# Kernel optimization log

Measured on AMD Instinct MI355X. Metric: run time of the kernel, lower is better.

The kernel has to match this reference:

```python
import jax, jax.numpy as jnp
import numpy as np

B, S, D, H, L = 256, 2048, 64, 256, 2


def setup_inputs() -> dict:
    key = jax.random.key(0)
    ks = jax.random.split(key, 12)
    s_in = 1.0 / np.sqrt(H)  # torch nn.RNN init bound
    inp = {
        "x": jax.random.normal(ks[0], (B, S, D), dtype=jnp.float32),
        "W_ih0": jax.random.uniform(ks[1], (H, D), jnp.float32, -s_in, s_in),
        "W_hh0": jax.random.uniform(ks[2], (H, H), jnp.float32, -s_in, s_in),
        "b_ih0": jax.random.uniform(ks[3], (H,), jnp.float32, -s_in, s_in),
        "b_hh0": jax.random.uniform(ks[4], (H,), jnp.float32, -s_in, s_in),
        "W_ih1": jax.random.uniform(ks[5], (H, H), jnp.float32, -s_in, s_in),
        "W_hh1": jax.random.uniform(ks[6], (H, H), jnp.float32, -s_in, s_in),
        "b_ih1": jax.random.uniform(ks[7], (H,), jnp.float32, -s_in, s_in),
        "b_hh1": jax.random.uniform(ks[8], (H,), jnp.float32, -s_in, s_in),
        "W_out": jax.random.uniform(ks[9], (1, H), jnp.float32, -s_in, s_in),
        "b_out": jax.random.uniform(ks[10], (1,), jnp.float32, -s_in, s_in),
    }
    return inp


def _rnn_layer_seq(xs, W_ih, W_hh, b_ih, b_hh):
    """xs: [S,B,Din] -> outputs [S,B,H]; collects every step."""
    # precompute input projection once (batched GEMM), recurrence only adds h @ W_hh
    pre = jnp.einsum('sbd,hd->sbh', xs, W_ih) + b_ih + b_hh  # [S,B,H]
    h0 = jnp.zeros((xs.shape[1], W_hh.shape[0]), dtype=xs.dtype)

    def step(h, p_t):
        h_new = jnp.tanh(p_t + h @ W_hh.T)
        return h_new, h_new

    _, ys = jax.lax.scan(step, h0, pre)
    return ys


def _rnn_layer_last(xs, W_ih, W_hh, b_ih, b_hh):
    """xs: [S,B,Din] -> final hidden state [B,H]; no per-step outputs kept."""
    pre = jnp.einsum('sbd,hd->sbh', xs, W_ih) + b_ih + b_hh
    h0 = jnp.zeros((xs.shape[1], W_hh.shape[0]), dtype=xs.dtype)

    def step(h, p_t):
        return jnp.tanh(p_t + h @ W_hh.T), None

    h_last, _ = jax.lax.scan(step, h0, pre)
    return h_last


def reference(x, W_ih0, W_hh0, b_ih0, b_hh0, W_ih1, W_hh1, b_ih1, b_hh1, W_out, b_out):
    xs = jnp.transpose(x, (1, 0, 2))  # [S,B,D] time-major for scan
    ys0 = _rnn_layer_seq(xs, W_ih0, W_hh0, b_ih0, b_hh0)      # [S,B,H]
    h_last = _rnn_layer_last(ys0, W_ih1, W_hh1, b_ih1, b_hh1)  # [B,H]
    return jax.nn.sigmoid(h_last @ W_out.T + b_out)            # [B,1]
```

## Files before the change

### kernel.cpp

```cpp
#include <hip/hip_runtime.h>
#include <cstdint>


#define S_LEN 2048
#define DIN   64
#define HDIM  256
#define CH    64

typedef __attribute__((ext_vector_type(8))) short bf16x8;
typedef __attribute__((ext_vector_type(4))) float f32x4;

__device__ __forceinline__ short f2bf(float f) {
  unsigned u = __builtin_bit_cast(unsigned, f);
  u += 0x7FFFu + ((u >> 16) & 1u);
  return (short)(u >> 16);
}
__device__ __forceinline__ float bf2f(unsigned short h) {
  return __builtin_bit_cast(float, ((unsigned)h) << 16);
}
__device__ __forceinline__ bf16x8 cvt8(f32x4 a, f32x4 b) {
  bf16x8 r;
  r[0]=f2bf(a[0]); r[1]=f2bf(a[1]); r[2]=f2bf(a[2]); r[3]=f2bf(a[3]);
  r[4]=f2bf(b[0]); r[5]=f2bf(b[1]); r[6]=f2bf(b[2]); r[7]=f2bf(b[3]);
  return r;
}
__device__ __forceinline__ bf16x8 load8cvt(const float* p) {
  f32x4 a = *(const f32x4*)p;
  f32x4 b = *(const f32x4*)(p + 4);
  return cvt8(a, b);
}
__device__ __forceinline__ f32x4 mfma16(bf16x8 a, bf16x8 b, f32x4 c) {
  return __builtin_amdgcn_mfma_f32_16x16x32_bf16(a, b, c, 0, 0, 0);
}
__device__ __forceinline__ float fast_tanh(float x) {
  float e = __expf(2.0f * x);
  float r = __builtin_amdgcn_rcpf(1.0f + e);
  return 1.0f - 2.0f * r;
}
__device__ __forceinline__ int frag_off(int k, int m) {
  return ((k >> 5) << 10) | (((k >> 3) & 3) << 8) | (m << 4) | ((k & 7) << 1);
}
__device__ __forceinline__ f32x4 unpk4(uint2 v) {
  f32x4 a;
  a[0] = __builtin_bit_cast(float, v.x << 16);
  a[1] = __builtin_bit_cast(float, v.x & 0xFFFF0000u);
  a[2] = __builtin_bit_cast(float, v.y << 16);
  a[3] = __builtin_bit_cast(float, v.y & 0xFFFF0000u);
  return a;
}
__device__ __forceinline__ uint2 pk4(f32x4 a) {
  uint2 p;
  p.x = (unsigned)(unsigned short)f2bf(a[0]) | ((unsigned)(unsigned short)f2bf(a[1]) << 16);
  p.y = (unsigned)(unsigned short)f2bf(a[2]) | ((unsigned)(unsigned short)f2bf(a[3]) << 16);
  return p;
}
__device__ __forceinline__ unsigned ld_acq(unsigned* p) {
  return __hip_atomic_load(p, __ATOMIC_ACQUIRE, __HIP_MEMORY_SCOPE_AGENT);
}
__device__ __forceinline__ void st_rlx(unsigned* p, unsigned v) {
  __hip_atomic_store(p, v, __ATOMIC_RELAXED, __HIP_MEMORY_SCOPE_AGENT);
}
__device__ __forceinline__ void bar_lds() {
  asm volatile("s_waitcnt lgkmcnt(0)" ::: "memory");
  __builtin_amdgcn_s_barrier();
}

__global__ void zero_flags(unsigned* f) {
  if (threadIdx.x < 64) f[threadIdx.x] = 0u;
}

__global__ void __launch_bounds__(256)
x_proj(const float* __restrict__ x, const float* __restrict__ Wih0,
       const float* __restrict__ bih0, const float* __restrict__ bhh0,
       uint2* __restrict__ pre0) {
  const int tid = threadIdx.x, w = tid >> 6, l = tid & 63;
  const int lm = l & 15, lq = l >> 4;
  const int tile = blockIdx.x, tch = blockIdx.y;

  bf16x8 wih[4][2]; float bias[4];
#pragma unroll
  for (int i = 0; i < 4; ++i) {
    int n = ((w * 4 + i) << 4) + lm;
    wih[i][0] = load8cvt(Wih0 + n * DIN + lq * 8);
    wih[i][1] = load8cvt(Wih0 + n * DIN + 32 + lq * 8);
    bias[i] = bih0[n] + bhh0[n];
  }
  const float* xb = x + (size_t)(tile * 16 + lm) * (S_LEN * DIN) + lq * 8;
  for (int tt = 0; tt < 16; ++tt) {
    int t = tch * 16 + tt;
    const float* xp = xb + (size_t)t * DIN;
    bf16x8 xa0 = load8cvt(xp);
    bf16x8 xa1 = load8cvt(xp + 32);
    uint2* dst = pre0 + ((size_t)(tile * S_LEN + t) * 16 + w * 4) * 64 + l;
#pragma unroll
    for (int i = 0; i < 4; ++i) {
      f32x4 a = {bias[i], bias[i], bias[i], bias[i]};
      a = mfma16(xa0, wih[i][0], a);
      a = mfma16(xa1, wih[i][1], a);
      dst[(size_t)i * 64] = pk4(a);
    }
  }
}

__global__ void __launch_bounds__(512, 2)
rnn_pipe2(const float* __restrict__ Whh0, const float* __restrict__ Wih1,
          const float* __restrict__ Whh1, const float* __restrict__ bih1,
          const float* __restrict__ bhh1, const float* __restrict__ Wout,
          const float* __restrict__ bout, uint2* __restrict__ pre0,
          unsigned* __restrict__ flags, float* __restrict__ out) {
  __shared__ __align__(16) char smem[17408];

  const int tid = threadIdx.x, w = tid >> 6, l = tid & 63;
  const int lm = l & 15, lq = l >> 4;
  const int role = blockIdx.x >> 4;
  const int tile = blockIdx.x & 15;

  const int lbase = l << 4;
  const int wbase = frag_off(w * 32 + lm, lq << 2);
  uint2* pb = pre0 + (size_t)tile * (S_LEN * 1024) + w * 128 + l;
  unsigned* flag = flags + tile;

  if (role == 0) {
    bf16x8 whh0[2][8], wih1[2][8];
    float bias1[2];
#pragma unroll
    for (int i = 0; i < 2; ++i) {
      int n = ((w * 2 + i) << 4) + lm;
#pragma unroll
      for (int kt = 0; kt < 8; ++kt) {
        whh0[i][kt] = load8cvt(Whh0 + n * HDIM + kt * 32 + lq * 8);
        wih1[i][kt] = load8cvt(Wih1 + n * HDIM + kt * 32 + lq * 8);
      }
      bias1[i] = bih1[n] + bhh1[n];
    }
    uint2 bufA[2], bufB[2];
    bufA[0] = pb[0];    bufA[1] = pb[64];
    bufB[0] = pb[1024]; bufB[1] = pb[1024 + 64];

    {
#pragma unroll
      for (int i = 0; i < 2; ++i) {
        f32x4 a = unpk4(bufA[i]);
#pragma unroll
        for (int r = 0; r < 4; ++r)
          *(short*)(smem + wbase + i * 512 + r * 16) = f2bf(fast_tanh(a[r]));
      }
      const uint2* np = pb + (size_t)2 * 1024;
      bufA[0] = np[0]; bufA[1] = np[64];
      bar_lds();
    }

    auto phaseA = [&](int p, int pbit, uint2 (&buf)[2]) {
      const int h0r = (pbit ^ 1) * 8192;
      const int h0w = pbit * 8192;
      f32x4 a0 = unpk4(buf[0]), a1 = unpk4(buf[1]);
      f32x4 g0 = {bias1[0], bias1[0], bias1[0], bias1[0]};
      f32x4 g1 = {bias1[1], bias1[1], bias1[1], bias1[1]};
#pragma unroll
      for (int kt = 0; kt < 8; ++kt) {
        bf16x8 hf = *(const bf16x8*)(smem + h0r + kt * 1024 + lbase);
        a0 = mfma16(hf, whh0[0][kt], a0);
        a1 = mfma16(hf, whh0[1][kt], a1);
        g0 = mfma16(hf, wih1[0][kt], g0);
        g1 = mfma16(hf, wih1[1][kt], g1);
      }
      {
        int tn = (p + 2 < S_LEN) ? p + 2 : S_LEN - 1;
        const uint2* np = pb + (size_t)tn * 1024;
        buf[0] = np[0]; buf[1] = np[64];
      }
#pragma unroll
      for (int i = 0; i < 2; ++i) {
        f32x4 a = i ? a1 : a0;
#pragma unroll
        for (int r = 0; r < 4; ++r)
          *(short*)(smem + h0w + wbase + i * 512 + r * 16) = f2bf(fast_tanh(a[r]));
      }
      {
        uint2* gd = pb + (size_t)(p - 1) * 1024;
        gd[0] = pk4(g0); gd[64] = pk4(g1);
      }
      if ((p & (CH - 1)) == 0) {
        __builtin_amdgcn_fence(__ATOMIC_RELEASE, "agent");
        __syncthreads();
        if (tid == 0) st_rlx(flag, (unsigned)(p >> 6));
      } else {
        bar_lds();
      }
    };

    for (int p = 1; p + 1 < S_LEN; p += 2) {
      phaseA(p, 1, bufB);
      phaseA(p + 1, 0, bufA);
    }
    phaseA(S_LEN - 1, 1, bufB);

    {
      f32x4 g0 = {bias1[0], bias1[0], bias1[0], bias1[0]};
      f32x4 g1 = {bias1[1], bias1[1], bias1[1], bias1[1]};
#pragma unroll
      for (int kt = 0; kt < 8; ++kt) {
        bf16x8 hf = *(const bf16x8*)(smem + 8192 + kt * 1024 + lbase);
        g0 = mfma16(hf, wih1[0][kt], g0);
        g1 = mfma16(hf, wih1[1][kt], g1);
      }
      uint2* gd = pb + (size_t)(S_LEN - 1) * 1024;
      gd[0] = pk4(g0); gd[64] = pk4(g1);
      __builtin_amdgcn_fence(__ATOMIC_RELEASE, "agent");
      __syncthreads();
      if (tid == 0) st_rlx(flag, (unsigned)(S_LEN / CH));
    }

  } else {
    bf16x8 whh1[2][8];
#pragma unroll
    for (int i = 0; i < 2; ++i) {
      int n = ((w * 2 + i) << 4) + lm;
#pragma unroll
      for (int kt = 0; kt < 8; ++kt)
        whh1[i][kt] = load8cvt(Whh1 + n * HDIM + kt * 32 + lq * 8);
    }
    ((f32x4*)(smem + 8192))[tid] = (f32x4){0.f, 0.f, 0.f, 0.f};
    __syncthreads();

    uint2 gcur[2], gnxt[2];
    unsigned have = 0;

    auto stepB = [&](int t, int pbit) {
      const int h1r = (pbit ^ 1) * 8192;
      const int h1w = pbit * 8192;
      const bool pf = ((t & (CH - 1)) != CH - 1);
      if (pf) {
        const uint2* np = pb + (size_t)(t + 1) * 1024;
        gnxt[0] = np[0]; gnxt[1] = np[64];
      }
      f32x4 c0 = unpk4(gcur[0]), c1 = unpk4(gcur[1]);
#pragma unroll
      for (int kt = 0; kt < 8; ++kt) {
        bf16x8 hf = *(const bf16x8*)(smem + h1r + kt * 1024 + lbase);
        c0 = mfma16(hf, whh1[0][kt], c0);
        c1 = mfma16(hf, whh1[1][kt], c1);
      }
#pragma unroll
      for (int i = 0; i < 2; ++i) {
        f32x4 c = i ? c1 : c0;
#pragma unroll
        for (int r = 0; r < 4; ++r)
          *(short*)(smem + h1w + wbase + i * 512 + r * 16) = f2bf(fast_tanh(c[r]));
      }
      if (pf) { gcur[0] = gnxt[0]; gcur[1] = gnxt[1]; }
      bar_lds();
    };

    for (int c = 0; c < S_LEN / CH; ++c) {
      while (have < (unsigned)(c + 1)) {
        have = ld_acq(flag);
        if (have < (unsigned)(c + 1)) __builtin_amdgcn_s_sleep(8);
      }
      const int t0 = c * CH;
      { const uint2* np = pb + (size_t)t0 * 1024; gcur[0] = np[0]; gcur[1] = np[64]; }
      for (int tt = 0; tt < CH; tt += 2) {
        stepB(t0 + tt, 0);
        stepB(t0 + tt + 1, 1);
      }
    }

    if (tid < 256) {
      int m = tid >> 4, j = tid & 15;
      float s = 0.f;
#pragma unroll
      for (int kk = 0; kk < 16; ++kk) {
        int k = j * 16 + kk;
        s += bf2f(*(unsigned short*)(smem + 8192 + frag_off(k, m))) * Wout[k];
      }
      ((float*)(smem + 16384))[(m << 4) + j] = s;
    }
    __syncthreads();
    if (tid < 16) {
      float s = 0.f;
#pragma unroll
      for (int j = 0; j < 16; ++j) s += ((float*)(smem + 16384))[(tid << 4) + j];
      s += bout[0];
      out[(tile << 4) + tid] = 1.f / (1.f + __expf(-s));
    }
  }
}

__global__ void __launch_bounds__(512, 2)
rnn_pre8(const float* __restrict__ Whh0, const float* __restrict__ Wih1,
         const float* __restrict__ Whh1, const float* __restrict__ bih1,
         const float* __restrict__ bhh1, const float* __restrict__ Wout,
         const float* __restrict__ bout, const uint2* __restrict__ pre0,
         float* __restrict__ out) {
  __shared__ __align__(16) char smem[33792];

  const int tid = threadIdx.x, w = tid >> 6, l = tid & 63;
  const int lm = l & 15, lq = l >> 4;
  const int tile = blockIdx.x;

  bf16x8 whh0[2][8], wih1[2][8], whh1[2][8];
  float bias1[2];
#pragma unroll
  for (int i = 0; i < 2; ++i) {
    int n = ((w * 2 + i) << 4) + lm;
#pragma unroll
    for (int kt = 0; kt < 8; ++kt) {
      whh0[i][kt] = load8cvt(Whh0 + n * HDIM + kt * 32 + lq * 8);
      wih1[i][kt] = load8cvt(Wih1 + n * HDIM + kt * 32 + lq * 8);
      whh1[i][kt] = load8cvt(Whh1 + n * HDIM + kt * 32 + lq * 8);
    }
    bias1[i] = bih1[n] + bhh1[n];
  }
  ((f32x4*)(smem + 24576))[tid] = (f32x4){0.f, 0.f, 0.f, 0.f};

  const int lbase = l << 4;
  const int wbase = frag_off(w * 32 + lm, lq << 2);
  const uint2* pbase = pre0 + (size_t)tile * (S_LEN * 1024) + w * 128 + l;
  uint2 bufA[2], bufB[2];
  bufA[0] = pbase[0];    bufA[1] = pbase[64];
  bufB[0] = pbase[1024]; bufB[1] = pbase[1024 + 64];

  {
#pragma unroll
    for (int i = 0; i < 2; ++i) {
      f32x4 a = unpk4(bufA[i]);
#pragma unroll
      for (int r = 0; r < 4; ++r)
        *(short*)(smem + wbase + i * 512 + r * 16) = f2bf(fast_tanh(a[r]));
    }
    const uint2* np = pbase + (size_t)2 * 1024;
    bufA[0] = np[0]; bufA[1] = np[64];
    bar_lds();
  }

  auto phase = [&](int p, int pbit, uint2 (&buf)[2]) {
    const int h0r_o = (pbit ^ 1) * 8192;
    const int h0w_o = pbit * 8192;
    const int h1r_o = 16384 + pbit * 8192;
    const int h1w_o = 16384 + (pbit ^ 1) * 8192;

    f32x4 a0 = unpk4(buf[0]), a1 = unpk4(buf[1]);
    f32x4 c0 = {bias1[0], bias1[0], bias1[0], bias1[0]};
    f32x4 c1 = {bias1[1], bias1[1], bias1[1], bias1[1]};
#pragma unroll
    for (int kt = 0; kt < 8; ++kt) {
      bf16x8 hf = *(const bf16x8*)(smem + h0r_o + kt * 1024 + lbase);
      a0 = mfma16(hf, whh0[0][kt], a0);
      a1 = mfma16(hf, whh0[1][kt], a1);
      c0 = mfma16(hf, wih1[0][kt], c0);
      c1 = mfma16(hf, wih1[1][kt], c1);
    }
#pragma unroll
    for (int kt = 0; kt < 8; ++kt) {
      bf16x8 hf = *(const bf16x8*)(smem + h1r_o + kt * 1024 + lbase);
      c0 = mfma16(hf, whh1[0][kt], c0);
      c1 = mfma16(hf, whh1[1][kt], c1);
    }
#pragma unroll
    for (int i = 0; i < 2; ++i) {
      f32x4 a = i ? a1 : a0;
      f32x4 c = i ? c1 : c0;
#pragma unroll
      for (int r = 0; r < 4; ++r) {
        *(short*)(smem + h0w_o + wbase + i * 512 + r * 16) = f2bf(fast_tanh(a[r]));
        *(short*)(smem + h1w_o + wbase + i * 512 + r * 16) = f2bf(fast_tanh(c[r]));
      }
    }
    {
      int tn = (p + 2 < S_LEN) ? p + 2 : S_LEN - 1;
      const uint2* np = pbase + (size_t)tn * 1024;
      buf[0] = np[0]; buf[1] = np[64];
    }
    bar_lds();
  };

  for (int p = 1; p + 1 < S_LEN; p += 2) {
    phase(p, 1, bufB);
    phase(p + 1, 0, bufA);
  }
  phase(S_LEN - 1, 1, bufB);

  {
    f32x4 c0 = {bias1[0], bias1[0], bias1[0], bias1[0]};
    f32x4 c1 = {bias1[1], bias1[1], bias1[1], bias1[1]};
#pragma unroll
    for (int kt = 0; kt < 8; ++kt) {
      bf16x8 hf = *(const bf16x8*)(smem + 8192 + kt * 1024 + lbase);
      c0 = mfma16(hf, wih1[0][kt], c0);
      c1 = mfma16(hf, wih1[1][kt], c1);
    }
#pragma unroll
    for (int kt = 0; kt < 8; ++kt) {
      bf16x8 hf = *(const bf16x8*)(smem + 16384 + kt * 1024 + lbase);
      c0 = mfma16(hf, whh1[0][kt], c0);
      c1 = mfma16(hf, whh1[1][kt], c1);
    }
#pragma unroll
    for (int i = 0; i < 2; ++i) {
      f32x4 c = i ? c1 : c0;
#pragma unroll
      for (int r = 0; r < 4; ++r)
        *(short*)(smem + 24576 + wbase + i * 512 + r * 16) = f2bf(fast_tanh(c[r]));
    }
    __syncthreads();
  }

  if (tid < 256) {
    int m = tid >> 4, j = tid & 15;
    float s = 0.f;
#pragma unroll
    for (int kk = 0; kk < 16; ++kk) {
      int k = j * 16 + kk;
      s += bf2f(*(unsigned short*)(smem + 24576 + frag_off(k, m))) * Wout[k];
    }
    ((float*)(smem + 32768))[(m << 4) + j] = s;
  }
  __syncthreads();
  if (tid < 16) {
    float s = 0.f;
#pragma unroll
    for (int j = 0; j < 16; ++j) s += ((float*)(smem + 32768))[(tid << 4) + j];
    s += bout[0];
    out[(tile << 4) + tid] = 1.f / (1.f + __expf(-s));
  }
}

extern "C" void kernel_launch(void* const* d_in, const int* in_sizes, int n_in,
                              void* d_out, int out_size, void* d_ws, size_t ws_size,
                              hipStream_t stream) {
  (void)in_sizes; (void)n_in; (void)out_size;
  const float* x    = (const float*)d_in[0];
  const float* Wih0 = (const float*)d_in[1];
  const float* Whh0 = (const float*)d_in[2];
  const float* bih0 = (const float*)d_in[3];
  const float* bhh0 = (const float*)d_in[4];
  const float* Wih1 = (const float*)d_in[5];
  const float* Whh1 = (const float*)d_in[6];
  const float* bih1 = (const float*)d_in[7];
  const float* bhh1 = (const float*)d_in[8];
  const float* Wout = (const float*)d_in[9];
  const float* bout = (const float*)d_in[10];

  const size_t PRE_BYTES = (size_t)16 * S_LEN * 16 * 64 * 8;

  x_proj<<<dim3(16, 128), dim3(256), 0, stream>>>(x, Wih0, bih0, bhh0,
                                                  (uint2*)d_ws);
  if (ws_size >= PRE_BYTES + 4096) {
    unsigned* flags = (unsigned*)((char*)d_ws + PRE_BYTES);
    zero_flags<<<dim3(1), dim3(64), 0, stream>>>(flags);
    rnn_pipe2<<<dim3(32), dim3(512), 0, stream>>>(
        Whh0, Wih1, Whh1, bih1, bhh1, Wout, bout, (uint2*)d_ws, flags,
        (float*)d_out);
  } else {
    rnn_pre8<<<dim3(16), dim3(512), 0, stream>>>(
        Whh0, Wih1, Whh1, bih1, bhh1, Wout, bout, (const uint2*)d_ws,
        (float*)d_out);
  }
}
```

Before: 2.166 ms.

## Halve waves per recurrent block, four output tiles per wave, packed DPP stores

The recurrent pipeline kernel now runs 4 waves of 256 threads instead of 8, and each wave computes four 16-column output tiles per step. Fewer waves per block should make each per-step barrier cheaper and raise MFMA work per wave. The cost is twice the register-resident weights, up to 64 bf16x8 fragments in the layer-0 role. Hidden-state stores to LDS now pair neighbouring lanes through DPP into 32-bit writes, and the consumer spin-wait gains an iteration budget that proceeds anyway once exhausted, which could read unready data.

```diff
diff --git a/kernel.cpp b/kernel.cpp
--- a/kernel.cpp
+++ b/kernel.cpp
@@ -36,6 +36,12 @@
   float e = __expf(2.0f * x);
   float r = __builtin_amdgcn_rcpf(1.0f + e);
   return 1.0f - 2.0f * r;
+}
+__device__ __forceinline__ f32x4 tanh4(f32x4 a) {
+  f32x4 r;
+  r[0] = fast_tanh(a[0]); r[1] = fast_tanh(a[1]);
+  r[2] = fast_tanh(a[2]); r[3] = fast_tanh(a[3]);
+  return r;
 }
 __device__ __forceinline__ int frag_off(int k, int m) {
   return ((k >> 5) << 10) | (((k >> 3) & 3) << 8) | (m << 4) | ((k & 7) << 1);
@@ -64,6 +70,15 @@
   asm volatile("s_waitcnt lgkmcnt(0)" ::: "memory");
   __builtin_amdgcn_s_barrier();
 }
+__device__ __forceinline__ void sth4(char* base, int wb, f32x4 a, int l) {
+#pragma unroll
+  for (int r = 0; r < 4; ++r) {
+    unsigned own = (unsigned)(unsigned short)f2bf(a[r]);
+    unsigned nb = (unsigned)__builtin_amdgcn_mov_dpp((int)own, 0xB1, 0xF, 0xF, true);
+    if ((l & 1) == 0)
+      *(unsigned*)(base + wb + r * 16) = own | (nb << 16);
+  }
+}
 
 __global__ void zero_flags(unsigned* f) {
   if (threadIdx.x < 64) f[threadIdx.x] = 0u;
@@ -102,8 +117,8 @@
   }
 }
 
-__global__ void __launch_bounds__(512, 2)
-rnn_pipe2(const float* __restrict__ Whh0, const float* __restrict__ Wih1,
+__global__ void __launch_bounds__(256, 1)
+rnn_pipe4(const float* __restrict__ Whh0, const float* __restrict__ Wih1,
           const float* __restrict__ Whh1, const float* __restrict__ bih1,
           const float* __restrict__ bhh1, const float* __restrict__ Wout,
           const float* __restrict__ bout, uint2* __restrict__ pre0,
@@ -116,69 +131,75 @@
   const int tile = blockIdx.x & 15;
 
   const int lbase = l << 4;
-  const int wbase = frag_off(w * 32 + lm, lq << 2);
-  uint2* pb = pre0 + (size_t)tile * (S_LEN * 1024) + w * 128 + l;
+  int wb[4];
+#pragma unroll
+  for (int i = 0; i < 4; ++i) wb[i] = frag_off(w * 64 + i * 16 + lm, lq << 2);
+  uint2* pb = pre0 + (size_t)tile * (S_LEN * 1024) + w * 256 + l;
   unsigned* flag = flags + tile;
 
   if (role == 0) {
-    bf16x8 whh0[2][8], wih1[2][8];
-    float bias1[2];
-#pragma unroll
-    for (int i = 0; i < 2; ++i) {
-      int n = ((w * 2 + i) << 4) + lm;
+    bf16x8 whh0[4][8], wih1r[4][8];
+    float bias1[4];
+#pragma unroll
+    for (int i = 0; i < 4; ++i) {
+      int n = ((w * 4 + i) << 4) + lm;
 #pragma unroll
       for (int kt = 0; kt < 8; ++kt) {
-        whh0[i][kt] = load8cvt(Whh0 + n * HDIM + kt * 32 + lq * 8);
-        wih1[i][kt] = load8cvt(Wih1 + n * HDIM + kt * 32 + lq * 8);
+        whh0[i][kt]  = load8cvt(Whh0 + n * HDIM + kt * 32 + lq * 8);
+        wih1r[i][kt] = load8cvt(Wih1 + n * HDIM + kt * 32 + lq * 8);
       }
       bias1[i] = bih1[n] + bhh1[n];
     }
-    uint2 bufA[2], bufB[2];
-    bufA[0] = pb[0];    bufA[1] = pb[64];
-    bufB[0] = pb[1024]; bufB[1] = pb[1024 + 64];
+    uint2 bufA[4], bufB[4];
+#pragma unroll
+    for (int i = 0; i < 4; ++i) {
+      bufA[i] = pb[i * 64];
+      bufB[i] = pb[1024 + i * 64];
+    }
 
     {
 #pragma unroll
-      for (int i = 0; i < 2; ++i) {
-        f32x4 a = unpk4(bufA[i]);
-#pragma unroll
-        for (int r = 0; r < 4; ++r)
-          *(short*)(smem + wbase + i * 512 + r * 16) = f2bf(fast_tanh(a[r]));
-      }
+      for (int i = 0; i < 4; ++i) sth4(smem, wb[i], tanh4(unpk4(bufA[i])), l);
       const uint2* np = pb + (size_t)2 * 1024;
-      bufA[0] = np[0]; bufA[1] = np[64];
+#pragma unroll
+      for (int i = 0; i < 4; ++i) bufA[i] = np[i * 64];
       bar_lds();
     }
 
-    auto phaseA = [&](int p, int pbit, uint2 (&buf)[2]) {
+    auto phaseA = [&](int p, int pbit, uint2 (&buf)[4]) {
       const int h0r = (pbit ^ 1) * 8192;
       const int h0w = pbit * 8192;
       f32x4 a0 = unpk4(buf[0]), a1 = unpk4(buf[1]);
+      f32x4 a2 = unpk4(buf[2]), a3 = unpk4(buf[3]);
       f32x4 g0 = {bias1[0], bias1[0], bias1[0], bias1[0]};
       f32x4 g1 = {bias1[1], bias1[1], bias1[1], bias1[1]};
+      f32x4 g2 = {bias1[2], bias1[2], bias1[2], bias1[2]};
+      f32x4 g3 = {bias1[3], bias1[3], bias1[3], bias1[3]};
 #pragma unroll
       for (int kt = 0; kt < 8; ++kt) {
         bf16x8 hf = *(const bf16x8*)(smem + h0r + kt * 1024 + lbase);
         a0 = mfma16(hf, whh0[0][kt], a0);
         a1 = mfma16(hf, whh0[1][kt], a1);
-        g0 = mfma16(hf, wih1[0][kt], g0);
-        g1 = mfma16(hf, wih1[1][kt], g1);
+        a2 = mfma16(hf, whh0[2][kt], a2);
+        a3 = mfma16(hf, whh0[3][kt], a3);
+        g0 = mfma16(hf, wih1r[0][kt], g0);
+        g1 = mfma16(hf, wih1r[1][kt], g1);
+        g2 = mfma16(hf, wih1r[2][kt], g2);
+        g3 = mfma16(hf, wih1r[3][kt], g3);
       }
       {
         int tn = (p + 2 < S_LEN) ? p + 2 : S_LEN - 1;
         const uint2* np = pb + (size_t)tn * 1024;
-        buf[0] = np[0]; buf[1] = np[64];
-      }
-#pragma unroll
-      for (int i = 0; i < 2; ++i) {
-        f32x4 a = i ? a1 : a0;
-#pragma unroll
-        for (int r = 0; r < 4; ++r)
-          *(short*)(smem + h0w + wbase + i * 512 + r * 16) = f2bf(fast_tanh(a[r]));
-      }
+#pragma unroll
+        for (int i = 0; i < 4; ++i) buf[i] = np[i * 64];
+      }
+      sth4(smem + h0w, wb[0], tanh4(a0), l);
+      sth4(smem + h0w, wb[1], tanh4(a1), l);
+      sth4(smem + h0w, wb[2], tanh4(a2), l);
+      sth4(smem + h0w, wb[3], tanh4(a3), l);
       {
         uint2* gd = pb + (size_t)(p - 1) * 1024;
-        gd[0] = pk4(g0); gd[64] = pk4(g1);
+        gd[0] = pk4(g0); gd[64] = pk4(g1); gd[128] = pk4(g2); gd[192] = pk4(g3);
       }
       if ((p & (CH - 1)) == 0) {
         __builtin_amdgcn_fence(__ATOMIC_RELEASE, "agent");
@@ -198,33 +219,39 @@
     {
       f32x4 g0 = {bias1[0], bias1[0], bias1[0], bias1[0]};
       f32x4 g1 = {bias1[1], bias1[1], bias1[1], bias1[1]};
+      f32x4 g2 = {bias1[2], bias1[2], bias1[2], bias1[2]};
+      f32x4 g3 = {bias1[3], bias1[3], bias1[3], bias1[3]};
 #pragma unroll
       for (int kt = 0; kt < 8; ++kt) {
         bf16x8 hf = *(const bf16x8*)(smem + 8192 + kt * 1024 + lbase);
-        g0 = mfma16(hf, wih1[0][kt], g0);
-        g1 = mfma16(hf, wih1[1][kt], g1);
+        g0 = mfma16(hf, wih1r[0][kt], g0);
+        g1 = mfma16(hf, wih1r[1][kt], g1);
+        g2 = mfma16(hf, wih1r[2][kt], g2);
+        g3 = mfma16(hf, wih1r[3][kt], g3);
       }
       uint2* gd = pb + (size_t)(S_LEN - 1) * 1024;
-      gd[0] = pk4(g0); gd[64] = pk4(g1);
+      gd[0] = pk4(g0); gd[64] = pk4(g1); gd[128] = pk4(g2); gd[192] = pk4(g3);
       __builtin_amdgcn_fence(__ATOMIC_RELEASE, "agent");
       __syncthreads();
       if (tid == 0) st_rlx(flag, (unsigned)(S_LEN / CH));
     }
 
   } else {
-    bf16x8 whh1[2][8];
-#pragma unroll
-    for (int i = 0; i < 2; ++i) {
-      int n = ((w * 2 + i) << 4) + lm;
+    bf16x8 whh1r[4][8];
+#pragma unroll
+    for (int i = 0; i < 4; ++i) {
+      int n = ((w * 4 + i) << 4) + lm;
 #pragma unroll
       for (int kt = 0; kt < 8; ++kt)
-        whh1[i][kt] = load8cvt(Whh1 + n * HDIM + kt * 32 + lq * 8);
+        whh1r[i][kt] = load8cvt(Whh1 + n * HDIM + kt * 32 + lq * 8);
     }
     ((f32x4*)(smem + 8192))[tid] = (f32x4){0.f, 0.f, 0.f, 0.f};
+    ((f32x4*)(smem + 8192))[tid + 256] = (f32x4){0.f, 0.f, 0.f, 0.f};
     __syncthreads();
 
-    uint2 gcur[2], gnxt[2];
+    uint2 gcur[4], gnxt[4];
     unsigned have = 0;
+    unsigned spin_budget = 4000000u;
 
     auto stepB = [&](int t, int pbit) {
       const int h1r = (pbit ^ 1) * 8192;
@@ -232,40 +259,51 @@
       const bool pf = ((t & (CH - 1)) != CH - 1);
       if (pf) {
         const uint2* np = pb + (size_t)(t + 1) * 1024;
-        gnxt[0] = np[0]; gnxt[1] = np[64];
+#pragma unroll
+        for (int i = 0; i < 4; ++i) gnxt[i] = np[i * 64];
       }
       f32x4 c0 = unpk4(gcur[0]), c1 = unpk4(gcur[1]);
+      f32x4 c2 = unpk4(gcur[2]), c3 = unpk4(gcur[3]);
 #pragma unroll
       for (int kt = 0; kt < 8; ++kt) {
         bf16x8 hf = *(const bf16x8*)(smem + h1r + kt * 1024 + lbase);
-        c0 = mfma16(hf, whh1[0][kt], c0);
-        c1 = mfma16(hf, whh1[1][kt], c1);
-      }
-#pragma unroll
-      for (int i = 0; i < 2; ++i) {
-        f32x4 c = i ? c1 : c0;
-#pragma unroll
-        for (int r = 0; r < 4; ++r)
-          *(short*)(smem + h1w + wbase + i * 512 + r * 16) = f2bf(fast_tanh(c[r]));
-      }
-      if (pf) { gcur[0] = gnxt[0]; gcur[1] = gnxt[1]; }
+        c0 = mfma16(hf, whh1r[0][kt], c0);
+        c1 = mfma16(hf, whh1r[1][kt], c1);
+        c2 = mfma16(hf, whh1r[2][kt], c2);
+        c3 = mfma16(hf, whh1r[3][kt], c3);
+      }
+      sth4(smem + h1w, wb[0], tanh4(c0), l);
+      sth4(smem + h1w, wb[1], tanh4(c1), l);
+      sth4(smem + h1w, wb[2], tanh4(c2), l);
+      sth4(smem + h1w, wb[3], tanh4(c3), l);
+      if (pf) {
+#pragma unroll
+        for (int i = 0; i < 4; ++i) gcur[i] = gnxt[i];
+      }
       bar_lds();
     };
 
     for (int c = 0; c < S_LEN / CH; ++c) {
       while (have < (unsigned)(c + 1)) {
         have = ld_acq(flag);
-        if (have < (unsigned)(c + 1)) __builtin_amdgcn_s_sleep(8);
+        if (have < (unsigned)(c + 1)) {
+          __builtin_amdgcn_s_sleep(8);
+          if (--spin_budget == 0u) { have = (unsigned)(c + 1); }
+        }
       }
       const int t0 = c * CH;
-      { const uint2* np = pb + (size_t)t0 * 1024; gcur[0] = np[0]; gcur[1] = np[64]; }
+      {
+        const uint2* np = pb + (size_t)t0 * 1024;
+#pragma unroll
+        for (int i = 0; i < 4; ++i) gcur[i] = np[i * 64];
+      }
       for (int tt = 0; tt < CH; tt += 2) {
         stepB(t0 + tt, 0);
         stepB(t0 + tt + 1, 1);
       }
     }
 
-    if (tid < 256) {
+    {
       int m = tid >> 4, j = tid & 15;
       float s = 0.f;
 #pragma unroll
@@ -448,7 +486,7 @@
   if (ws_size >= PRE_BYTES + 4096) {
     unsigned* flags = (unsigned*)((char*)d_ws + PRE_BYTES);
     zero_flags<<<dim3(1), dim3(64), 0, stream>>>(flags);
-    rnn_pipe2<<<dim3(32), dim3(512), 0, stream>>>(
+    rnn_pipe4<<<dim3(32), dim3(256), 0, stream>>>(
         Whh0, Wih1, Whh1, bih1, bhh1, Wout, bout, (uint2*)d_ws, flags,
         (float*)d_out);
   } else {
```

New measurement: 3.550 ms. +63.9%, slower.

## Split layer-1 input projection into a third block role in pipelined RNN

Applied to the files above, without the earlier changes.

Layer-0 blocks no longer compute the W_ih1 projection inside their serial recurrence. They now write the bf16 hidden states to the workspace, and a new group of 16 blocks computes the layer-1 gate preactivations chunk by chunk, signalling layer-1 blocks through a second flag. LDS hidden-state stores are packed into 32-bit writes using DPP lane exchange. The aim is to shorten the per-step critical path of layer 0, at the cost of an extra pipeline stage, more global traffic, more blocks, and bounded spin waits that can fall through on timeout.

```diff
diff --git a/kernel.cpp b/kernel.cpp
--- a/kernel.cpp
+++ b/kernel.cpp
@@ -36,6 +36,12 @@
   float e = __expf(2.0f * x);
   float r = __builtin_amdgcn_rcpf(1.0f + e);
   return 1.0f - 2.0f * r;
+}
+__device__ __forceinline__ f32x4 tanh4(f32x4 a) {
+  f32x4 r;
+  r[0] = fast_tanh(a[0]); r[1] = fast_tanh(a[1]);
+  r[2] = fast_tanh(a[2]); r[3] = fast_tanh(a[3]);
+  return r;
 }
 __device__ __forceinline__ int frag_off(int k, int m) {
   return ((k >> 5) << 10) | (((k >> 3) & 3) << 8) | (m << 4) | ((k & 7) << 1);
@@ -64,6 +70,15 @@
   asm volatile("s_waitcnt lgkmcnt(0)" ::: "memory");
   __builtin_amdgcn_s_barrier();
 }
+__device__ __forceinline__ void sth4(char* base, int wb, f32x4 a, int l) {
+#pragma unroll
+  for (int r = 0; r < 4; ++r) {
+    unsigned own = (unsigned)(unsigned short)f2bf(a[r]);
+    unsigned nb = (unsigned)__builtin_amdgcn_mov_dpp((int)own, 0xB1, 0xF, 0xF, true);
+    if ((l & 1) == 0)
+      *(unsigned*)(base + wb + r * 16) = own | (nb << 16);
+  }
+}
 
 __global__ void zero_flags(unsigned* f) {
   if (threadIdx.x < 64) f[threadIdx.x] = 0u;
@@ -103,12 +118,12 @@
 }
 
 __global__ void __launch_bounds__(512, 2)
-rnn_pipe2(const float* __restrict__ Whh0, const float* __restrict__ Wih1,
-          const float* __restrict__ Whh1, const float* __restrict__ bih1,
-          const float* __restrict__ bhh1, const float* __restrict__ Wout,
-          const float* __restrict__ bout, uint2* __restrict__ pre0,
-          unsigned* __restrict__ flags, float* __restrict__ out) {
-  __shared__ __align__(16) char smem[17408];
+rnn_pipe3b(const float* __restrict__ Whh0, const float* __restrict__ Wih1,
+           const float* __restrict__ Whh1, const float* __restrict__ bih1,
+           const float* __restrict__ bhh1, const float* __restrict__ Wout,
+           const float* __restrict__ bout, uint2* __restrict__ pre0,
+           unsigned* __restrict__ flags, float* __restrict__ out) {
+  __shared__ __align__(16) char smem[33792];
 
   const int tid = threadIdx.x, w = tid >> 6, l = tid & 63;
   const int lm = l & 15, lq = l >> 4;
@@ -118,33 +133,26 @@
   const int lbase = l << 4;
   const int wbase = frag_off(w * 32 + lm, lq << 2);
   uint2* pb = pre0 + (size_t)tile * (S_LEN * 1024) + w * 128 + l;
-  unsigned* flag = flags + tile;
+  char* pgb = (char*)(pre0 + (size_t)tile * (S_LEN * 1024));
+  unsigned* flagA = flags + tile;
+  unsigned* flagG = flags + 16 + tile;
 
   if (role == 0) {
-    bf16x8 whh0[2][8], wih1[2][8];
-    float bias1[2];
+    bf16x8 whh0[2][8];
 #pragma unroll
     for (int i = 0; i < 2; ++i) {
       int n = ((w * 2 + i) << 4) + lm;
 #pragma unroll
-      for (int kt = 0; kt < 8; ++kt) {
+      for (int kt = 0; kt < 8; ++kt)
         whh0[i][kt] = load8cvt(Whh0 + n * HDIM + kt * 32 + lq * 8);
-        wih1[i][kt] = load8cvt(Wih1 + n * HDIM + kt * 32 + lq * 8);
-      }
-      bias1[i] = bih1[n] + bhh1[n];
     }
     uint2 bufA[2], bufB[2];
     bufA[0] = pb[0];    bufA[1] = pb[64];
     bufB[0] = pb[1024]; bufB[1] = pb[1024 + 64];
 
     {
-#pragma unroll
-      for (int i = 0; i < 2; ++i) {
-        f32x4 a = unpk4(bufA[i]);
-#pragma unroll
-        for (int r = 0; r < 4; ++r)
-          *(short*)(smem + wbase + i * 512 + r * 16) = f2bf(fast_tanh(a[r]));
-      }
+      sth4(smem, wbase, tanh4(unpk4(bufA[0])), l);
+      sth4(smem, wbase + 512, tanh4(unpk4(bufA[1])), l);
       const uint2* np = pb + (size_t)2 * 1024;
       bufA[0] = np[0]; bufA[1] = np[64];
       bar_lds();
@@ -153,37 +161,26 @@
     auto phaseA = [&](int p, int pbit, uint2 (&buf)[2]) {
       const int h0r = (pbit ^ 1) * 8192;
       const int h0w = pbit * 8192;
+      char* hst = pgb + (size_t)(p - 1) * 8192 + w * 1024 + lbase;
       f32x4 a0 = unpk4(buf[0]), a1 = unpk4(buf[1]);
-      f32x4 g0 = {bias1[0], bias1[0], bias1[0], bias1[0]};
-      f32x4 g1 = {bias1[1], bias1[1], bias1[1], bias1[1]};
 #pragma unroll
       for (int kt = 0; kt < 8; ++kt) {
         bf16x8 hf = *(const bf16x8*)(smem + h0r + kt * 1024 + lbase);
         a0 = mfma16(hf, whh0[0][kt], a0);
         a1 = mfma16(hf, whh0[1][kt], a1);
-        g0 = mfma16(hf, wih1[0][kt], g0);
-        g1 = mfma16(hf, wih1[1][kt], g1);
+        if (kt == w) *(bf16x8*)hst = hf;
       }
       {
         int tn = (p + 2 < S_LEN) ? p + 2 : S_LEN - 1;
         const uint2* np = pb + (size_t)tn * 1024;
         buf[0] = np[0]; buf[1] = np[64];
       }
-#pragma unroll
-      for (int i = 0; i < 2; ++i) {
-        f32x4 a = i ? a1 : a0;
-#pragma unroll
-        for (int r = 0; r < 4; ++r)
-          *(short*)(smem + h0w + wbase + i * 512 + r * 16) = f2bf(fast_tanh(a[r]));
-      }
-      {
-        uint2* gd = pb + (size_t)(p - 1) * 1024;
-        gd[0] = pk4(g0); gd[64] = pk4(g1);
-      }
+      sth4(smem + h0w, wbase, tanh4(a0), l);
+      sth4(smem + h0w, wbase + 512, tanh4(a1), l);
       if ((p & (CH - 1)) == 0) {
         __builtin_amdgcn_fence(__ATOMIC_RELEASE, "agent");
         __syncthreads();
-        if (tid == 0) st_rlx(flag, (unsigned)(p >> 6));
+        if (tid == 0) st_rlx(flagA, (unsigned)(p >> 6));
       } else {
         bar_lds();
       }
@@ -196,35 +193,83 @@
     phaseA(S_LEN - 1, 1, bufB);
 
     {
-      f32x4 g0 = {bias1[0], bias1[0], bias1[0], bias1[0]};
-      f32x4 g1 = {bias1[1], bias1[1], bias1[1], bias1[1]};
-#pragma unroll
-      for (int kt = 0; kt < 8; ++kt) {
-        bf16x8 hf = *(const bf16x8*)(smem + 8192 + kt * 1024 + lbase);
-        g0 = mfma16(hf, wih1[0][kt], g0);
-        g1 = mfma16(hf, wih1[1][kt], g1);
-      }
-      uint2* gd = pb + (size_t)(S_LEN - 1) * 1024;
-      gd[0] = pk4(g0); gd[64] = pk4(g1);
+      bf16x8 hf = *(const bf16x8*)(smem + 8192 + w * 1024 + lbase);
+      *(bf16x8*)(pgb + (size_t)(S_LEN - 1) * 8192 + w * 1024 + lbase) = hf;
       __builtin_amdgcn_fence(__ATOMIC_RELEASE, "agent");
       __syncthreads();
-      if (tid == 0) st_rlx(flag, (unsigned)(S_LEN / CH));
-    }
-
-  } else {
-    bf16x8 whh1[2][8];
+      if (tid == 0) st_rlx(flagA, (unsigned)(S_LEN / CH));
+    }
+
+  } else if (role == 1) {
+    bf16x8 wih1g[2][8];
+    float bias1[2];
 #pragma unroll
     for (int i = 0; i < 2; ++i) {
       int n = ((w * 2 + i) << 4) + lm;
 #pragma unroll
       for (int kt = 0; kt < 8; ++kt)
-        whh1[i][kt] = load8cvt(Whh1 + n * HDIM + kt * 32 + lq * 8);
+        wih1g[i][kt] = load8cvt(Wih1 + n * HDIM + kt * 32 + lq * 8);
+      bias1[i] = bih1[n] + bhh1[n];
+    }
+    unsigned have = 0;
+    unsigned budget = 4000000u;
+    const int sslot = w >> 1, sq = w & 1;
+
+    for (int c = 0; c < S_LEN / CH; ++c) {
+      while (have < (unsigned)(c + 1)) {
+        have = ld_acq(flagA);
+        if (have < (unsigned)(c + 1)) {
+          __builtin_amdgcn_s_sleep(8);
+          if (--budget == 0u) { have = (unsigned)(c + 1); }
+        }
+      }
+      for (int bs = 0; bs < CH / 4; ++bs) {
+        const int t0 = c * CH + bs * 4;
+        {
+          const char* src = pgb + (size_t)(t0 + sslot) * 8192 + sq * 4096 + lbase;
+          char* dst = smem + sslot * 8192 + sq * 4096 + lbase;
+#pragma unroll
+          for (int kk = 0; kk < 4; ++kk) {
+            bf16x8 v = *(const bf16x8*)(src + kk * 1024);
+            *(bf16x8*)(dst + kk * 1024) = v;
+          }
+        }
+        bar_lds();
+#pragma unroll
+        for (int s = 0; s < 4; ++s) {
+          f32x4 c0 = {bias1[0], bias1[0], bias1[0], bias1[0]};
+          f32x4 c1 = {bias1[1], bias1[1], bias1[1], bias1[1]};
+#pragma unroll
+          for (int kt = 0; kt < 8; ++kt) {
+            bf16x8 hf = *(const bf16x8*)(smem + s * 8192 + kt * 1024 + lbase);
+            c0 = mfma16(hf, wih1g[0][kt], c0);
+            c1 = mfma16(hf, wih1g[1][kt], c1);
+          }
+          uint2* gd = pb + (size_t)(t0 + s) * 1024;
+          gd[0] = pk4(c0); gd[64] = pk4(c1);
+        }
+        bar_lds();
+      }
+      __builtin_amdgcn_fence(__ATOMIC_RELEASE, "agent");
+      __syncthreads();
+      if (tid == 0) st_rlx(flagG, (unsigned)(c + 1));
+    }
+
+  } else {
+    bf16x8 whh1r[2][8];
+#pragma unroll
+    for (int i = 0; i < 2; ++i) {
+      int n = ((w * 2 + i) << 4) + lm;
+#pragma unroll
+      for (int kt = 0; kt < 8; ++kt)
+        whh1r[i][kt] = load8cvt(Whh1 + n * HDIM + kt * 32 + lq * 8);
     }
     ((f32x4*)(smem + 8192))[tid] = (f32x4){0.f, 0.f, 0.f, 0.f};
     __syncthreads();
 
     uint2 gcur[2], gnxt[2];
     unsigned have = 0;
+    unsigned budget = 4000000u;
 
     auto stepB = [&](int t, int pbit) {
       const int h1r = (pbit ^ 1) * 8192;
@@ -238,24 +283,22 @@
 #pragma unroll
       for (int kt = 0; kt < 8; ++kt) {
         bf16x8 hf = *(const bf16x8*)(smem + h1r + kt * 1024 + lbase);
-        c0 = mfma16(hf, whh1[0][kt], c0);
-        c1 = mfma16(hf, whh1[1][kt], c1);
-      }
-#pragma unroll
-      for (int i = 0; i < 2; ++i) {
-        f32x4 c = i ? c1 : c0;
-#pragma unroll
-        for (int r = 0; r < 4; ++r)
-          *(short*)(smem + h1w + wbase + i * 512 + r * 16) = f2bf(fast_tanh(c[r]));
-      }
+        c0 = mfma16(hf, whh1r[0][kt], c0);
+        c1 = mfma16(hf, whh1r[1][kt], c1);
+      }
+      sth4(smem + h1w, wbase, tanh4(c0), l);
+      sth4(smem + h1w, wbase + 512, tanh4(c1), l);
       if (pf) { gcur[0] = gnxt[0]; gcur[1] = gnxt[1]; }
       bar_lds();
     };
 
     for (int c = 0; c < S_LEN / CH; ++c) {
       while (have < (unsigned)(c + 1)) {
-        have = ld_acq(flag);
-        if (have < (unsigned)(c + 1)) __builtin_amdgcn_s_sleep(8);
+        have = ld_acq(flagG);
+        if (have < (unsigned)(c + 1)) {
+          __builtin_amdgcn_s_sleep(8);
+          if (--budget == 0u) { have = (unsigned)(c + 1); }
+        }
       }
       const int t0 = c * CH;
       { const uint2* np = pb + (size_t)t0 * 1024; gcur[0] = np[0]; gcur[1] = np[64]; }
@@ -448,7 +491,7 @@
   if (ws_size >= PRE_BYTES + 4096) {
     unsigned* flags = (unsigned*)((char*)d_ws + PRE_BYTES);
     zero_flags<<<dim3(1), dim3(64), 0, stream>>>(flags);
-    rnn_pipe2<<<dim3(32), dim3(512), 0, stream>>>(
+    rnn_pipe3b<<<dim3(48), dim3(512), 0, stream>>>(
         Whh0, Wih1, Whh1, bih1, bhh1, Wout, bout, (uint2*)d_ws, flags,
         (float*)d_out);
   } else {
```

After: 2.396 ms. 10.6% more time.
